# Kernel tuning notes

Hardware: AMD Instinct MI355X
Metric: run time of the kernel (lower is better)

The kernel has to match this reference:

```python
import jax, jax.numpy as jnp
from jax import lax
import numpy as np

B, N1, N2 = 4, 2048, 8192
C1, C2, K, F = 128, 64, 15, 128
NSAMPLE = 16
RADIUS = 0.2
KP_EXTEND = 1.0
EXTENT = KP_EXTEND * RADIUS  # area of influence of each kernel point


def setup_inputs() -> dict:
    key = jax.random.key(0)
    k0, k1, k2, k3, k4 = jax.random.split(key, 5)
    xyz1 = jax.random.uniform(k0, (B, N1, 3), dtype=jnp.float32)
    xyz2 = jax.random.uniform(k1, (B, N2, 3), dtype=jnp.float32)
    features1 = jax.random.normal(k2, (B, N1, C1), dtype=jnp.float32)
    features2 = jax.random.normal(k3, (B, N2, C2), dtype=jnp.float32)
    # Kernel points: fixed disposition inside a sphere of RADIUS, first point at
    # center (fixed='center'). Stands in for the offline potential-optimization.
    rng = np.random.RandomState(42)
    dirs = rng.randn(K, 3)
    dirs /= (np.linalg.norm(dirs, axis=1, keepdims=True) + 1e-9)
    rad = rng.rand(K, 1) ** (1.0 / 3.0)
    kp = dirs * rad
    kp[0, :] = 0.0  # fixed center point
    kernel_points = jnp.asarray(kp * RADIUS, dtype=jnp.float32)  # (K, 3)
    # Convolution kernel weights: one C1->F matrix per kernel point.
    W = jax.random.normal(k4, (K, C1, F), dtype=jnp.float32) * 0.05
    return {"xyz1": xyz1, "features1": features1, "xyz2": xyz2,
            "features2": features2, "kernel_points": kernel_points, "W": W}


def reference(xyz1, features1, xyz2, features2, kernel_points, W):
    # kNN search: for each query point in set 2, NSAMPLE nearest points in set 1.
    d2 = jnp.sum((xyz2[:, :, None, :] - xyz1[:, None, :, :]) ** 2, axis=-1)  # (B,N2,N1)
    _, idx = lax.top_k(-d2, NSAMPLE)  # (B, N2, S)
    # Irregular gather of neighbor coordinates and features.
    gather = jax.vmap(lambda arr, i: arr[i])  # per-batch fancy gather
    neigh_xyz = gather(xyz1, idx)        # (B, N2, S, 3)
    neigh_feat = gather(features1, idx)  # (B, N2, S, C1)
    # Neighbor positions relative to the query (center) point.
    rel = neigh_xyz - xyz2[:, :, None, :]  # (B, N2, S, 3)
    # Distances from each neighbor to each kernel point.
    diff = rel[:, :, :, None, :] - kernel_points[None, None, None, :, :]  # (B,N2,S,K,3)
    sq = jnp.sum(diff * diff, axis=-1)                                    # (B,N2,S,K)
    dist = jnp.sqrt(jnp.maximum(sq, 1e-12))
    # Linear kernel-point influence, aggregation_mode='sum'.
    weights = jax.nn.relu(1.0 - dist / EXTENT)  # (B, N2, S, K)
    # Weighted aggregation of neighbor features per kernel point.
    wf = jnp.einsum('bnsk,bnsc->bnkc', weights, neigh_feat)  # (B, N2, K, C1)
    # Kernel point convolution: per-kernel-point linear map, summed over K.
    out = jnp.einsum('bnkc,kcf->bnf', wf, W)  # (B, N2, F)
    out = jax.nn.relu(out)
    # Feature propagation: concat with skip features of set 2 (use_xyz=False).
    return jnp.concatenate([out, features2], axis=-1)  # (B, N2, F + C2)
```

## Files before the change

### kernel.cpp

```cpp
#include <hip/hip_runtime.h>

#define B 4
#define N1 2048
#define N2 8192
#define C1 128
#define C2 64
#define K 15
#define F 128
#define S 16

__global__ __launch_bounds__(512) void knn_kernel(
    const float* __restrict__ xyz1, const float* __restrict__ xyz2,
    unsigned short* __restrict__ nn_idx) {
#pragma clang fp contract(off)
  __shared__ float sx[N1], sy[N1], sz[N1];
  __shared__ float s_cd[16][522];
  __shared__ unsigned short s_ci[16][522];
  const int b = blockIdx.y;
  const int q0 = blockIdx.x * 16;
  const int tid = threadIdx.x;

  const float* p1 = xyz1 + (size_t)b * N1 * 3;
  for (int i = tid; i < N1; i += 512) {
    sx[i] = p1[i * 3 + 0];
    sy[i] = p1[i * 3 + 1];
    sz[i] = p1[i * 3 + 2];
  }
  __syncthreads();

  const int wv = tid >> 6;
  const int lane = tid & 63;
  const int q = lane & 15;
  const int sub = lane >> 4;
  const float* p2 = xyz2 + ((size_t)b * N2 + q0 + q) * 3;
  const float qx = p2[0], qy = p2[1], qz = p2[2];

  float bd[S];
  int bi[S];
#pragma unroll
  for (int j = 0; j < S; ++j) { bd[j] = 3.4e38f; bi[j] = 0x7fffffff; }

  const int i0 = wv * 256 + sub;
  for (int ii = 0; ii < 64; ++ii) {
    const int i = i0 + (ii << 2);
    float dx = qx - sx[i];
    float dy = qy - sy[i];
    float dz = qz - sz[i];
    float d = dx * dx;
    d = d + dy * dy;
    d = d + dz * dz;
    if (d < bd[S - 1]) {
      bd[S - 1] = d;
      bi[S - 1] = i;
#pragma unroll
      for (int j = S - 1; j > 0; --j) {
        if (bd[j] < bd[j - 1]) {
          float td = bd[j]; bd[j] = bd[j - 1]; bd[j - 1] = td;
          int ti = bi[j]; bi[j] = bi[j - 1]; bi[j - 1] = ti;
        }
      }
    }
  }
  {
    const int ls = (wv * 4 + sub) * 16;
#pragma unroll
    for (int j = 0; j < S; ++j) {
      s_cd[q][ls + j] = bd[j];
      s_ci[q][ls + j] = (unsigned short)bi[j];
    }
  }
  __syncthreads();

  for (int L = 32; L >= 4; L >>= 1) {
    const int half = L >> 1;
    const int nact = 16 * half;
    const int valid = tid < nact;
    float od[16];
    int oi[16];
    int q2 = 0, m = 0;
    if (valid) {
      q2 = tid / half;
      m = tid - q2 * half;
      int pa = (2 * m) * 16, ea = pa + 16;
      int pb = ea, eb = pb + 16;
#pragma unroll
      for (int j = 0; j < 16; ++j) {
        const int a_ok = pa < ea, b_ok = pb < eb;
        const int ra = a_ok ? pa : ea - 1;
        const int rb = b_ok ? pb : eb - 1;
        float da = s_cd[q2][ra];
        int ia = (int)s_ci[q2][ra];
        float db = s_cd[q2][rb];
        int ib = (int)s_ci[q2][rb];
        const int ta = a_ok && (!b_ok || da < db || (da == db && ia < ib));
        od[j] = ta ? da : db;
        oi[j] = ta ? ia : ib;
        pa += ta;
        pb += !ta;
      }
    }
    __syncthreads();
    if (valid) {
#pragma unroll
      for (int j = 0; j < 16; ++j) {
        s_cd[q2][m * 16 + j] = od[j];
        s_ci[q2][m * 16 + j] = (unsigned short)oi[j];
      }
    }
    __syncthreads();
  }

  if (tid < 16) {
    const int q2 = tid;
    int pa = 0, ea = 16, pb = 16, eb = 32;
    unsigned short* op = nn_idx + ((size_t)b * N2 + q0 + q2) * S;
#pragma unroll
    for (int j = 0; j < 16; ++j) {
      const int a_ok = pa < ea, b_ok = pb < eb;
      const int ra = a_ok ? pa : ea - 1;
      const int rb = b_ok ? pb : eb - 1;
      float da = s_cd[q2][ra];
      int ia = (int)s_ci[q2][ra];
      float db = s_cd[q2][rb];
      int ib = (int)s_ci[q2][rb];
      const int ta = a_ok && (!b_ok || da < db || (da == db && ia < ib));
      op[j] = (unsigned short)(ta ? ia : ib);
      pa += ta;
      pb += !ta;
    }
  }
}

__global__ __launch_bounds__(256) void conv_kernel(
    const float* __restrict__ xyz1, const float* __restrict__ feat1,
    const float* __restrict__ xyz2, const float* __restrict__ feat2,
    const float* __restrict__ kp, const float* __restrict__ W,
    const unsigned short* __restrict__ nn_idx, float* __restrict__ out) {
  __shared__ __align__(16) float s_buf[8448];
  int (*s_idx)[S] = (int(*)[S])(s_buf);
  float (*s_rel)[S][3] = (float(*)[S][3])(s_buf + 256);
  float (*s_w)[260] = (float(*)[260])(s_buf + 1024);
  float (*s_red)[16][132] = (float(*)[16][132])(s_buf);
  __shared__ float s_wf[C1][20];
  __shared__ float s_kp[K * 3];

  const int b = blockIdx.y;
  const int q0 = blockIdx.x * 16;
  const int tid = threadIdx.x;

  if (tid < K * 3) s_kp[tid] = kp[tid];
  s_idx[tid >> 4][tid & 15] = (int)nn_idx[((size_t)b * N2 + q0) * S + tid];
  __syncthreads();

  {
    int q = tid >> 4, s = tid & 15;
    int i = s_idx[q][s];
    const float* pn = xyz1 + ((size_t)b * N1 + i) * 3;
    const float* pq = xyz2 + ((size_t)b * N2 + q0 + q) * 3;
    s_rel[q][s][0] = pn[0] - pq[0];
    s_rel[q][s][1] = pn[1] - pq[1];
    s_rel[q][s][2] = pn[2] - pq[2];
  }
  __syncthreads();

  for (int t = tid; t < 16 * S * K; t += 256) {
    int q = t / (S * K);
    int r = t - q * (S * K);
    int s = r / K;
    int k = r - s * K;
    float rx = s_rel[q][s][0] - s_kp[k * 3 + 0];
    float ry = s_rel[q][s][1] - s_kp[k * 3 + 1];
    float rz = s_rel[q][s][2] - s_kp[k * 3 + 2];
    float d = sqrtf(fmaxf(rx * rx + ry * ry + rz * rz, 1e-12f));
    s_w[q][s * 16 + k] = fmaxf(0.0f, 1.0f - d / 0.2f);
  }
  __syncthreads();

  const int q = tid & 15;
  const int cg = tid >> 4;

  float wfr[K][8];
#pragma unroll
  for (int k = 0; k < K; ++k)
#pragma unroll
    for (int j = 0; j < 8; ++j) wfr[k][j] = 0.0f;

  for (int s = 0; s < S; ++s) {
    int i = s_idx[q][s];
    const float4* fp = (const float4*)(feat1 + ((size_t)b * N1 + i) * C1) + cg * 2;
    float4 n0 = fp[0];
    float4 n1 = fp[1];
    const float4* wr = (const float4*)(&s_w[q][s * 16]);
    float4 w0 = wr[0], w1 = wr[1], w2 = wr[2], w3 = wr[3];
    float wk[16] = {w0.x, w0.y, w0.z, w0.w, w1.x, w1.y, w1.z, w1.w,
                    w2.x, w2.y, w2.z, w2.w, w3.x, w3.y, w3.z, w3.w};
#pragma unroll
    for (int k = 0; k < K; ++k) {
      float w = wk[k];
      wfr[k][0] += w * n0.x;
      wfr[k][1] += w * n0.y;
      wfr[k][2] += w * n0.z;
      wfr[k][3] += w * n0.w;
      wfr[k][4] += w * n1.x;
      wfr[k][5] += w * n1.y;
      wfr[k][6] += w * n1.z;
      wfr[k][7] += w * n1.w;
    }
  }

  const int qg = tid >> 7;
  const int cs = (tid >> 5) & 3;
  const int fg = tid & 31;
  float4 acc[8];
#pragma unroll
  for (int qi = 0; qi < 8; ++qi) acc[qi] = make_float4(0.f, 0.f, 0.f, 0.f);

  for (int k = 0; k < K; ++k) {
    __syncthreads();
#pragma unroll
    for (int j = 0; j < 8; ++j) s_wf[cg * 8 + j][q] = wfr[k][j];
    __syncthreads();

    const float4* Wk4 = (const float4*)(W + (size_t)k * C1 * F) + fg;
#pragma unroll 4
    for (int c2 = 0; c2 < 32; ++c2) {
      int c = cs * 32 + c2;
      float4 wa = *(const float4*)(&s_wf[c][qg * 8 + 0]);
      float4 wb = *(const float4*)(&s_wf[c][qg * 8 + 4]);
      float4 w4 = Wk4[c * 32];
      acc[0].x += wa.x * w4.x; acc[0].y += wa.x * w4.y;
      acc[0].z += wa.x * w4.z; acc[0].w += wa.x * w4.w;
      acc[1].x += wa.y * w4.x; acc[1].y += wa.y * w4.y;
      acc[1].z += wa.y * w4.z; acc[1].w += wa.y * w4.w;
      acc[2].x += wa.z * w4.x; acc[2].y += wa.z * w4.y;
      acc[2].z += wa.z * w4.z; acc[2].w += wa.z * w4.w;
      acc[3].x += wa.w * w4.x; acc[3].y += wa.w * w4.y;
      acc[3].z += wa.w * w4.z; acc[3].w += wa.w * w4.w;
      acc[4].x += wb.x * w4.x; acc[4].y += wb.x * w4.y;
      acc[4].z += wb.x * w4.z; acc[4].w += wb.x * w4.w;
      acc[5].x += wb.y * w4.x; acc[5].y += wb.y * w4.y;
      acc[5].z += wb.y * w4.z; acc[5].w += wb.y * w4.w;
      acc[6].x += wb.z * w4.x; acc[6].y += wb.z * w4.y;
      acc[6].z += wb.z * w4.z; acc[6].w += wb.z * w4.w;
      acc[7].x += wb.w * w4.x; acc[7].y += wb.w * w4.y;
      acc[7].z += wb.w * w4.z; acc[7].w += wb.w * w4.w;
    }
  }

#pragma unroll
  for (int qi = 0; qi < 8; ++qi)
    *(float4*)(&s_red[cs][qg * 8 + qi][fg * 4]) = acc[qi];
  __syncthreads();

  for (int t = tid; t < 512; t += 256) {
    int qq = t >> 5;
    int fj = t & 31;
    float4 a0 = *(const float4*)&s_red[0][qq][fj * 4];
    float4 a1 = *(const float4*)&s_red[1][qq][fj * 4];
    float4 a2 = *(const float4*)&s_red[2][qq][fj * 4];
    float4 a3 = *(const float4*)&s_red[3][qq][fj * 4];
    float4 v;
    v.x = fmaxf(a0.x + a1.x + a2.x + a3.x, 0.0f);
    v.y = fmaxf(a0.y + a1.y + a2.y + a3.y, 0.0f);
    v.z = fmaxf(a0.z + a1.z + a2.z + a3.z, 0.0f);
    v.w = fmaxf(a0.w + a1.w + a2.w + a3.w, 0.0f);
    ((float4*)(out + ((size_t)b * N2 + q0 + qq) * (F + C2)))[fj] = v;
  }

  {
    int qq = tid >> 4;
    int j = tid & 15;
    float4 v = ((const float4*)(feat2 + ((size_t)b * N2 + q0 + qq) * C2))[j];
    ((float4*)(out + ((size_t)b * N2 + q0 + qq) * (F + C2) + F))[j] = v;
  }
}

extern "C" void kernel_launch(void* const* d_in, const int* in_sizes, int n_in,
                              void* d_out, int out_size, void* d_ws, size_t ws_size,
                              hipStream_t stream) {
  const float* xyz1 = (const float*)d_in[0];
  const float* feat1 = (const float*)d_in[1];
  const float* xyz2 = (const float*)d_in[2];
  const float* feat2 = (const float*)d_in[3];
  const float* kp = (const float*)d_in[4];
  const float* Wm = (const float*)d_in[5];
  float* out = (float*)d_out;

  unsigned short* nn_idx = (unsigned short*)d_ws;

  knn_kernel<<<dim3(N2 / 16, B), 512, 0, stream>>>(xyz1, xyz2, nn_idx);
  conv_kernel<<<dim3(N2 / 16, B), 256, 0, stream>>>(xyz1, feat1, xyz2, feat2,
                                                    kp, Wm, nn_idx, out);
}
```

Measured before the change: 550.2 us.

## Split kernel-point aggregation into two chunks and halve reduction shared memory

The conv kernel now builds the weighted neighbour features in two chunks of eight and seven kernel points, running the W projection for each chunk right after it, instead of holding all fifteen in registers. This cuts the live accumulator registers. The cross-thread reduction is staged in two passes through a buffer half the previous size, which shrinks the block's shared memory. Both changes aim to raise occupancy, at the cost of gathering the neighbour features twice and adding extra barriers.

```diff
diff --git a/kernel.cpp b/kernel.cpp
--- a/kernel.cpp
+++ b/kernel.cpp
@@ -136,7 +136,7 @@
     const float* __restrict__ xyz2, const float* __restrict__ feat2,
     const float* __restrict__ kp, const float* __restrict__ W,
     const unsigned short* __restrict__ nn_idx, float* __restrict__ out) {
-  __shared__ __align__(16) float s_buf[8448];
+  __shared__ __align__(16) float s_buf[5184];
   int (*s_idx)[S] = (int(*)[S])(s_buf);
   float (*s_rel)[S][3] = (float(*)[S][3])(s_buf + 256);
   float (*s_w)[260] = (float(*)[260])(s_buf + 1024);
@@ -178,93 +178,134 @@
 
   const int q = tid & 15;
   const int cg = tid >> 4;
-
-  float wfr[K][8];
-#pragma unroll
-  for (int k = 0; k < K; ++k)
-#pragma unroll
-    for (int j = 0; j < 8; ++j) wfr[k][j] = 0.0f;
-
-  for (int s = 0; s < S; ++s) {
-    int i = s_idx[q][s];
-    const float4* fp = (const float4*)(feat1 + ((size_t)b * N1 + i) * C1) + cg * 2;
-    float4 n0 = fp[0];
-    float4 n1 = fp[1];
-    const float4* wr = (const float4*)(&s_w[q][s * 16]);
-    float4 w0 = wr[0], w1 = wr[1], w2 = wr[2], w3 = wr[3];
-    float wk[16] = {w0.x, w0.y, w0.z, w0.w, w1.x, w1.y, w1.z, w1.w,
-                    w2.x, w2.y, w2.z, w2.w, w3.x, w3.y, w3.z, w3.w};
-#pragma unroll
-    for (int k = 0; k < K; ++k) {
-      float w = wk[k];
-      wfr[k][0] += w * n0.x;
-      wfr[k][1] += w * n0.y;
-      wfr[k][2] += w * n0.z;
-      wfr[k][3] += w * n0.w;
-      wfr[k][4] += w * n1.x;
-      wfr[k][5] += w * n1.y;
-      wfr[k][6] += w * n1.z;
-      wfr[k][7] += w * n1.w;
-    }
-  }
-
   const int qg = tid >> 7;
   const int cs = (tid >> 5) & 3;
   const int fg = tid & 31;
+
   float4 acc[8];
 #pragma unroll
   for (int qi = 0; qi < 8; ++qi) acc[qi] = make_float4(0.f, 0.f, 0.f, 0.f);
 
-  for (int k = 0; k < K; ++k) {
-    __syncthreads();
-#pragma unroll
-    for (int j = 0; j < 8; ++j) s_wf[cg * 8 + j][q] = wfr[k][j];
-    __syncthreads();
-
-    const float4* Wk4 = (const float4*)(W + (size_t)k * C1 * F) + fg;
+#pragma unroll
+  for (int chunk = 0; chunk < 2; ++chunk) {
+    const int kbase = chunk * 8;
+    const int kn = chunk ? 7 : 8;
+
+    float wfr[8][8];
+#pragma unroll
+    for (int kk = 0; kk < 8; ++kk)
+#pragma unroll
+      for (int j = 0; j < 8; ++j) wfr[kk][j] = 0.0f;
+
+    for (int s = 0; s < S; ++s) {
+      int i = s_idx[q][s];
+      const float4* fp =
+          (const float4*)(feat1 + ((size_t)b * N1 + i) * C1) + cg * 2;
+      float4 n0 = fp[0];
+      float4 n1 = fp[1];
+      const float4* wr = (const float4*)(&s_w[q][s * 16]);
+      float4 wa = wr[chunk * 2 + 0];
+      float4 wb = wr[chunk * 2 + 1];
+      float wk[8] = {wa.x, wa.y, wa.z, wa.w, wb.x, wb.y, wb.z, wb.w};
+#pragma unroll
+      for (int kk = 0; kk < 8; ++kk) {
+        if (kk < kn) {
+          float w = wk[kk];
+          wfr[kk][0] += w * n0.x;
+          wfr[kk][1] += w * n0.y;
+          wfr[kk][2] += w * n0.z;
+          wfr[kk][3] += w * n0.w;
+          wfr[kk][4] += w * n1.x;
+          wfr[kk][5] += w * n1.y;
+          wfr[kk][6] += w * n1.z;
+          wfr[kk][7] += w * n1.w;
+        }
+      }
+    }
+
+#pragma unroll
+    for (int kk = 0; kk < 8; ++kk) {
+      if (kk < kn) {
+        const int kg = kbase + kk;
+        __syncthreads();
+#pragma unroll
+        for (int j = 0; j < 8; ++j) s_wf[cg * 8 + j][q] = wfr[kk][j];
+        __syncthreads();
+
+        const float4* Wk4 = (const float4*)(W + (size_t)kg * C1 * F) + fg;
 #pragma unroll 4
-    for (int c2 = 0; c2 < 32; ++c2) {
-      int c = cs * 32 + c2;
-      float4 wa = *(const float4*)(&s_wf[c][qg * 8 + 0]);
-      float4 wb = *(const float4*)(&s_wf[c][qg * 8 + 4]);
-      float4 w4 = Wk4[c * 32];
-      acc[0].x += wa.x * w4.x; acc[0].y += wa.x * w4.y;
-      acc[0].z += wa.x * w4.z; acc[0].w += wa.x * w4.w;
-      acc[1].x += wa.y * w4.x; acc[1].y += wa.y * w4.y;
-      acc[1].z += wa.y * w4.z; acc[1].w += wa.y * w4.w;
-      acc[2].x += wa.z * w4.x; acc[2].y += wa.z * w4.y;
-      acc[2].z += wa.z * w4.z; acc[2].w += wa.z * w4.w;
-      acc[3].x += wa.w * w4.x; acc[3].y += wa.w * w4.y;
-      acc[3].z += wa.w * w4.z; acc[3].w += wa.w * w4.w;
-      acc[4].x += wb.x * w4.x; acc[4].y += wb.x * w4.y;
-      acc[4].z += wb.x * w4.z; acc[4].w += wb.x * w4.w;
-      acc[5].x += wb.y * w4.x; acc[5].y += wb.y * w4.y;
-      acc[5].z += wb.y * w4.z; acc[5].w += wb.y * w4.w;
-      acc[6].x += wb.z * w4.x; acc[6].y += wb.z * w4.y;
-      acc[6].z += wb.z * w4.z; acc[6].w += wb.z * w4.w;
-      acc[7].x += wb.w * w4.x; acc[7].y += wb.w * w4.y;
-      acc[7].z += wb.w * w4.z; acc[7].w += wb.w * w4.w;
-    }
-  }
-
-#pragma unroll
-  for (int qi = 0; qi < 8; ++qi)
-    *(float4*)(&s_red[cs][qg * 8 + qi][fg * 4]) = acc[qi];
-  __syncthreads();
-
-  for (int t = tid; t < 512; t += 256) {
-    int qq = t >> 5;
-    int fj = t & 31;
-    float4 a0 = *(const float4*)&s_red[0][qq][fj * 4];
-    float4 a1 = *(const float4*)&s_red[1][qq][fj * 4];
-    float4 a2 = *(const float4*)&s_red[2][qq][fj * 4];
-    float4 a3 = *(const float4*)&s_red[3][qq][fj * 4];
+        for (int c2 = 0; c2 < 32; ++c2) {
+          int c = cs * 32 + c2;
+          float4 wa = *(const float4*)(&s_wf[c][qg * 8 + 0]);
+          float4 wb = *(const float4*)(&s_wf[c][qg * 8 + 4]);
+          float4 w4 = Wk4[c * 32];
+          acc[0].x += wa.x * w4.x; acc[0].y += wa.x * w4.y;
+          acc[0].z += wa.x * w4.z; acc[0].w += wa.x * w4.w;
+          acc[1].x += wa.y * w4.x; acc[1].y += wa.y * w4.y;
+          acc[1].z += wa.y * w4.z; acc[1].w += wa.y * w4.w;
+          acc[2].x += wa.z * w4.x; acc[2].y += wa.z * w4.y;
+          acc[2].z += wa.z * w4.z; acc[2].w += wa.z * w4.w;
+          acc[3].x += wa.w * w4.x; acc[3].y += wa.w * w4.y;
+          acc[3].z += wa.w * w4.z; acc[3].w += wa.w * w4.w;
+          acc[4].x += wb.x * w4.x; acc[4].y += wb.x * w4.y;
+          acc[4].z += wb.x * w4.z; acc[4].w += wb.x * w4.w;
+          acc[5].x += wb.y * w4.x; acc[5].y += wb.y * w4.y;
+          acc[5].z += wb.y * w4.z; acc[5].w += wb.y * w4.w;
+          acc[6].x += wb.z * w4.x; acc[6].y += wb.z * w4.y;
+          acc[6].z += wb.z * w4.z; acc[6].w += wb.z * w4.w;
+          acc[7].x += wb.w * w4.x; acc[7].y += wb.w * w4.y;
+          acc[7].z += wb.w * w4.z; acc[7].w += wb.w * w4.w;
+        }
+      }
+    }
+  }
+
+  const int qq0 = tid >> 5;
+  const int qq1 = 8 + (tid >> 5);
+  const int fj = tid & 31;
+
+  if (cs < 2) {
+#pragma unroll
+    for (int qi = 0; qi < 8; ++qi)
+      *(float4*)(&s_red[cs][qg * 8 + qi][fg * 4]) = acc[qi];
+  }
+  __syncthreads();
+
+  float4 s01_0, s01_1;
+  {
+    float4 a0 = *(const float4*)&s_red[0][qq0][fj * 4];
+    float4 a1 = *(const float4*)&s_red[1][qq0][fj * 4];
+    s01_0.x = a0.x + a1.x; s01_0.y = a0.y + a1.y;
+    s01_0.z = a0.z + a1.z; s01_0.w = a0.w + a1.w;
+    float4 b0 = *(const float4*)&s_red[0][qq1][fj * 4];
+    float4 b1 = *(const float4*)&s_red[1][qq1][fj * 4];
+    s01_1.x = b0.x + b1.x; s01_1.y = b0.y + b1.y;
+    s01_1.z = b0.z + b1.z; s01_1.w = b0.w + b1.w;
+  }
+  __syncthreads();
+  if (cs >= 2) {
+#pragma unroll
+    for (int qi = 0; qi < 8; ++qi)
+      *(float4*)(&s_red[cs - 2][qg * 8 + qi][fg * 4]) = acc[qi];
+  }
+  __syncthreads();
+  {
+    float4 a2 = *(const float4*)&s_red[0][qq0][fj * 4];
+    float4 a3 = *(const float4*)&s_red[1][qq0][fj * 4];
     float4 v;
-    v.x = fmaxf(a0.x + a1.x + a2.x + a3.x, 0.0f);
-    v.y = fmaxf(a0.y + a1.y + a2.y + a3.y, 0.0f);
-    v.z = fmaxf(a0.z + a1.z + a2.z + a3.z, 0.0f);
-    v.w = fmaxf(a0.w + a1.w + a2.w + a3.w, 0.0f);
-    ((float4*)(out + ((size_t)b * N2 + q0 + qq) * (F + C2)))[fj] = v;
+    v.x = fmaxf((s01_0.x + a2.x) + a3.x, 0.0f);
+    v.y = fmaxf((s01_0.y + a2.y) + a3.y, 0.0f);
+    v.z = fmaxf((s01_0.z + a2.z) + a3.z, 0.0f);
+    v.w = fmaxf((s01_0.w + a2.w) + a3.w, 0.0f);
+    ((float4*)(out + ((size_t)b * N2 + q0 + qq0) * (F + C2)))[fj] = v;
+    float4 b2 = *(const float4*)&s_red[0][qq1][fj * 4];
+    float4 b3 = *(const float4*)&s_red[1][qq1][fj * 4];
+    float4 u;
+    u.x = fmaxf((s01_1.x + b2.x) + b3.x, 0.0f);
+    u.y = fmaxf((s01_1.y + b2.y) + b3.y, 0.0f);
+    u.z = fmaxf((s01_1.z + b2.z) + b3.z, 0.0f);
+    u.w = fmaxf((s01_1.w + b2.w) + b3.w, 0.0f);
+    ((float4*)(out + ((size_t)b * N2 + q0 + qq1) * (F + C2)))[fj] = u;
   }
 
   {
```

New measurement: 917.2 us. +66.7%, slower.

## Double conv block to 512 threads with double-buffered per-kernel-point staging

Applied to the files above, without the earlier changes.

The conv kernel now runs 512 threads per block. Each thread holds half the channels (4 instead of 8) in the aggregation stage and half the queries (4 instead of 8) in the kernel-point matmul, which cuts register pressure and doubles thread-level parallelism. The per-kernel-point shared staging buffer is double-buffered, so each iteration needs one barrier instead of two. The final reduction runs in two phases to fit a smaller shared buffer. In exchange, each W value is loaded by twice as many threads, giving more global/L2 traffic for W, and the extra reduction barriers add some overhead.

```diff
diff --git a/kernel.cpp b/kernel.cpp
--- a/kernel.cpp
+++ b/kernel.cpp
@@ -131,17 +131,17 @@
   }
 }
 
-__global__ __launch_bounds__(256) void conv_kernel(
+__global__ __launch_bounds__(512) void conv_kernel(
     const float* __restrict__ xyz1, const float* __restrict__ feat1,
     const float* __restrict__ xyz2, const float* __restrict__ feat2,
     const float* __restrict__ kp, const float* __restrict__ W,
     const unsigned short* __restrict__ nn_idx, float* __restrict__ out) {
-  __shared__ __align__(16) float s_buf[8448];
+  __shared__ __align__(16) float s_buf[5184];
   int (*s_idx)[S] = (int(*)[S])(s_buf);
   float (*s_rel)[S][3] = (float(*)[S][3])(s_buf + 256);
   float (*s_w)[260] = (float(*)[260])(s_buf + 1024);
   float (*s_red)[16][132] = (float(*)[16][132])(s_buf);
-  __shared__ float s_wf[C1][20];
+  __shared__ float s_wf[2][C1][20];
   __shared__ float s_kp[K * 3];
 
   const int b = blockIdx.y;
@@ -149,10 +149,11 @@
   const int tid = threadIdx.x;
 
   if (tid < K * 3) s_kp[tid] = kp[tid];
-  s_idx[tid >> 4][tid & 15] = (int)nn_idx[((size_t)b * N2 + q0) * S + tid];
-  __syncthreads();
-
-  {
+  if (tid < 256)
+    s_idx[tid >> 4][tid & 15] = (int)nn_idx[((size_t)b * N2 + q0) * S + tid];
+  __syncthreads();
+
+  if (tid < 256) {
     int q = tid >> 4, s = tid & 15;
     int i = s_idx[q][s];
     const float* pn = xyz1 + ((size_t)b * N1 + i) * 3;
@@ -163,7 +164,7 @@
   }
   __syncthreads();
 
-  for (int t = tid; t < 16 * S * K; t += 256) {
+  for (int t = tid; t < 16 * S * K; t += 512) {
     int q = t / (S * K);
     int r = t - q * (S * K);
     int s = r / K;
@@ -179,17 +180,16 @@
   const int q = tid & 15;
   const int cg = tid >> 4;
 
-  float wfr[K][8];
+  float wfr[K][4];
 #pragma unroll
   for (int k = 0; k < K; ++k)
 #pragma unroll
-    for (int j = 0; j < 8; ++j) wfr[k][j] = 0.0f;
+    for (int j = 0; j < 4; ++j) wfr[k][j] = 0.0f;
 
   for (int s = 0; s < S; ++s) {
     int i = s_idx[q][s];
-    const float4* fp = (const float4*)(feat1 + ((size_t)b * N1 + i) * C1) + cg * 2;
+    const float4* fp = (const float4*)(feat1 + ((size_t)b * N1 + i) * C1) + cg;
     float4 n0 = fp[0];
-    float4 n1 = fp[1];
     const float4* wr = (const float4*)(&s_w[q][s * 16]);
     float4 w0 = wr[0], w1 = wr[1], w2 = wr[2], w3 = wr[3];
     float wk[16] = {w0.x, w0.y, w0.z, w0.w, w1.x, w1.y, w1.z, w1.w,
@@ -201,32 +201,32 @@
       wfr[k][1] += w * n0.y;
       wfr[k][2] += w * n0.z;
       wfr[k][3] += w * n0.w;
-      wfr[k][4] += w * n1.x;
-      wfr[k][5] += w * n1.y;
-      wfr[k][6] += w * n1.z;
-      wfr[k][7] += w * n1.w;
     }
   }
 
   const int qg = tid >> 7;
   const int cs = (tid >> 5) & 3;
   const int fg = tid & 31;
-  float4 acc[8];
-#pragma unroll
-  for (int qi = 0; qi < 8; ++qi) acc[qi] = make_float4(0.f, 0.f, 0.f, 0.f);
-
+  float4 acc[4];
+#pragma unroll
+  for (int qi = 0; qi < 4; ++qi) acc[qi] = make_float4(0.f, 0.f, 0.f, 0.f);
+
+#pragma unroll
+  for (int j = 0; j < 4; ++j) s_wf[0][cg * 4 + j][q] = wfr[0][j];
+  __syncthreads();
+
+#pragma unroll
   for (int k = 0; k < K; ++k) {
-    __syncthreads();
-#pragma unroll
-    for (int j = 0; j < 8; ++j) s_wf[cg * 8 + j][q] = wfr[k][j];
-    __syncthreads();
-
+    const int cur = k & 1;
+    if (k + 1 < K) {
+#pragma unroll
+      for (int j = 0; j < 4; ++j) s_wf[cur ^ 1][cg * 4 + j][q] = wfr[k + 1][j];
+    }
     const float4* Wk4 = (const float4*)(W + (size_t)k * C1 * F) + fg;
 #pragma unroll 4
     for (int c2 = 0; c2 < 32; ++c2) {
       int c = cs * 32 + c2;
-      float4 wa = *(const float4*)(&s_wf[c][qg * 8 + 0]);
-      float4 wb = *(const float4*)(&s_wf[c][qg * 8 + 4]);
+      float4 wa = *(const float4*)(&s_wf[cur][c][qg * 4]);
       float4 w4 = Wk4[c * 32];
       acc[0].x += wa.x * w4.x; acc[0].y += wa.x * w4.y;
       acc[0].z += wa.x * w4.z; acc[0].w += wa.x * w4.w;
@@ -236,42 +236,50 @@
       acc[2].z += wa.z * w4.z; acc[2].w += wa.z * w4.w;
       acc[3].x += wa.w * w4.x; acc[3].y += wa.w * w4.y;
       acc[3].z += wa.w * w4.z; acc[3].w += wa.w * w4.w;
-      acc[4].x += wb.x * w4.x; acc[4].y += wb.x * w4.y;
-      acc[4].z += wb.x * w4.z; acc[4].w += wb.x * w4.w;
-      acc[5].x += wb.y * w4.x; acc[5].y += wb.y * w4.y;
-      acc[5].z += wb.y * w4.z; acc[5].w += wb.y * w4.w;
-      acc[6].x += wb.z * w4.x; acc[6].y += wb.z * w4.y;
-      acc[6].z += wb.z * w4.z; acc[6].w += wb.z * w4.w;
-      acc[7].x += wb.w * w4.x; acc[7].y += wb.w * w4.y;
-      acc[7].z += wb.w * w4.z; acc[7].w += wb.w * w4.w;
-    }
-  }
-
-#pragma unroll
-  for (int qi = 0; qi < 8; ++qi)
-    *(float4*)(&s_red[cs][qg * 8 + qi][fg * 4]) = acc[qi];
-  __syncthreads();
-
-  for (int t = tid; t < 512; t += 256) {
-    int qq = t >> 5;
-    int fj = t & 31;
+    }
+    __syncthreads();
+  }
+
+  const int qq = tid >> 5;
+  const int fj = tid & 31;
+
+  if (cs < 2) {
+#pragma unroll
+    for (int qi = 0; qi < 4; ++qi)
+      *(float4*)(&s_red[cs][qg * 4 + qi][fg * 4]) = acc[qi];
+  }
+  __syncthreads();
+
+  float4 s01;
+  {
     float4 a0 = *(const float4*)&s_red[0][qq][fj * 4];
     float4 a1 = *(const float4*)&s_red[1][qq][fj * 4];
-    float4 a2 = *(const float4*)&s_red[2][qq][fj * 4];
-    float4 a3 = *(const float4*)&s_red[3][qq][fj * 4];
+    s01.x = a0.x + a1.x; s01.y = a0.y + a1.y;
+    s01.z = a0.z + a1.z; s01.w = a0.w + a1.w;
+  }
+  __syncthreads();
+  if (cs >= 2) {
+#pragma unroll
+    for (int qi = 0; qi < 4; ++qi)
+      *(float4*)(&s_red[cs - 2][qg * 4 + qi][fg * 4]) = acc[qi];
+  }
+  __syncthreads();
+  {
+    float4 a2 = *(const float4*)&s_red[0][qq][fj * 4];
+    float4 a3 = *(const float4*)&s_red[1][qq][fj * 4];
     float4 v;
-    v.x = fmaxf(a0.x + a1.x + a2.x + a3.x, 0.0f);
-    v.y = fmaxf(a0.y + a1.y + a2.y + a3.y, 0.0f);
-    v.z = fmaxf(a0.z + a1.z + a2.z + a3.z, 0.0f);
-    v.w = fmaxf(a0.w + a1.w + a2.w + a3.w, 0.0f);
+    v.x = fmaxf((s01.x + a2.x) + a3.x, 0.0f);
+    v.y = fmaxf((s01.y + a2.y) + a3.y, 0.0f);
+    v.z = fmaxf((s01.z + a2.z) + a3.z, 0.0f);
+    v.w = fmaxf((s01.w + a2.w) + a3.w, 0.0f);
     ((float4*)(out + ((size_t)b * N2 + q0 + qq) * (F + C2)))[fj] = v;
   }
 
-  {
-    int qq = tid >> 4;
+  if (tid < 256) {
+    int qq2 = tid >> 4;
     int j = tid & 15;
-    float4 v = ((const float4*)(feat2 + ((size_t)b * N2 + q0 + qq) * C2))[j];
-    ((float4*)(out + ((size_t)b * N2 + q0 + qq) * (F + C2) + F))[j] = v;
+    float4 v = ((const float4*)(feat2 + ((size_t)b * N2 + q0 + qq2) * C2))[j];
+    ((float4*)(out + ((size_t)b * N2 + q0 + qq2) * (F + C2) + F))[j] = v;
   }
 }
 
@@ -289,6 +297,6 @@
   unsigned short* nn_idx = (unsigned short*)d_ws;
 
   knn_kernel<<<dim3(N2 / 16, B), 512, 0, stream>>>(xyz1, xyz2, nn_idx);
-  conv_kernel<<<dim3(N2 / 16, B), 256, 0, stream>>>(xyz1, feat1, xyz2, feat2,
+  conv_kernel<<<dim3(N2 / 16, B), 512, 0, stream>>>(xyz1, feat1, xyz2, feat2,
                                                     kp, Wm, nn_idx, out);
 }
```

Measured after the change: 989.9 us. 79.9% more time.
